# Kernel tuning notes

Hardware: AMD Instinct MI355X
Metric: run time of the kernel (lower is better)

Reference implementation:

```python
import jax, jax.numpy as jnp
import numpy as np

HEADS = 8
DH = 160
LN_EPS = 1e-5


def _ln(x):
    m = jnp.mean(x, axis=-1, keepdims=True)
    v = jnp.var(x, axis=-1, keepdims=True)
    return (x - m) * jax.lax.rsqrt(v + LN_EPS)


def _adaln(x, table, w, b, t):
    # table[t]: [dim]; emb -> [2*dim]; chunk along dim 0 (scalar timestep)
    emb = jax.nn.silu(table[t]) @ w + b
    scale, shift = jnp.split(emb, 2)
    return _ln(x) * (1.0 + scale) + shift


def _attn(x, ctx, wq, wk, wv, wo, bo):
    B, S, _ = x.shape
    Sk = ctx.shape[1]
    q = (x @ wq).reshape(B, S, HEADS, DH).transpose(0, 2, 1, 3)    # [B,H,S,dh]
    k = (ctx @ wk).reshape(B, Sk, HEADS, DH).transpose(0, 2, 1, 3)
    v = (ctx @ wv).reshape(B, Sk, HEADS, DH).transpose(0, 2, 1, 3)
    scores = jnp.einsum('bhid,bhjd->bhij', q, k) * (DH ** -0.5)
    probs = jax.nn.softmax(scores, axis=-1)
    o = jnp.einsum('bhij,bhjd->bhid', probs, v)
    o = o.transpose(0, 2, 1, 3).reshape(B, S, HEADS * DH)
    return o @ wo + bo


def _ff(x, w1, b1, w2, b2):
    h, gate = jnp.split(x @ w1 + b1, 2, axis=-1)
    return (h * jax.nn.gelu(gate, approximate=False)) @ w2 + b2


def setup_inputs() -> dict:
    key = jax.random.key(0)
    ks = jax.random.split(key, 24)
    B, S, SC, DIM, CROSS, INNER = 2, 2048, 77, 1280, 768, 5120

    def w(k, shape, s=0.02):
        return jax.random.normal(k, shape, jnp.float32) * s

    return {
        'hidden_states': jax.random.normal(ks[0], (B, S, DIM), jnp.float32),
        'context': jax.random.normal(ks[1], (B, SC, CROSS), jnp.float32),
        'ada1_emb': w(ks[2], (1000, DIM)),
        'ada1_w': w(ks[3], (DIM, 2 * DIM)),
        'ada1_b': jnp.zeros((2 * DIM,), jnp.float32),
        'ada2_emb': w(ks[4], (1000, DIM)),
        'ada2_w': w(ks[5], (DIM, 2 * DIM)),
        'ada2_b': jnp.zeros((2 * DIM,), jnp.float32),
        'a1_wq': w(ks[6], (DIM, DIM)), 'a1_wk': w(ks[7], (DIM, DIM)),
        'a1_wv': w(ks[8], (DIM, DIM)), 'a1_wo': w(ks[9], (DIM, DIM)),
        'a1_bo': jnp.zeros((DIM,), jnp.float32),
        'a2_wq': w(ks[10], (DIM, DIM)), 'a2_wk': w(ks[11], (CROSS, DIM)),
        'a2_wv': w(ks[12], (CROSS, DIM)), 'a2_wo': w(ks[13], (DIM, DIM)),
        'a2_bo': jnp.zeros((DIM,), jnp.float32),
        'norm3_g': jnp.ones((DIM,), jnp.float32),
        'norm3_b': jnp.zeros((DIM,), jnp.float32),
        'ff_w1': w(ks[14], (DIM, 2 * INNER)),
        'ff_b1': jnp.zeros((2 * INNER,), jnp.float32),
        'ff_w2': w(ks[15], (INNER, DIM)),
        'ff_b2': jnp.zeros((DIM,), jnp.float32),
        'timestep': 500,
    }


def reference(hidden_states, context, ada1_emb, ada1_w, ada1_b, ada2_emb, ada2_w, ada2_b,
              a1_wq, a1_wk, a1_wv, a1_wo, a1_bo, a2_wq, a2_wk, a2_wv, a2_wo, a2_bo,
              norm3_g, norm3_b, ff_w1, ff_b1, ff_w2, ff_b2, timestep):
    x = hidden_states
    # self-attention with AdaLayerNorm
    h = _adaln(x, ada1_emb, ada1_w, ada1_b, timestep)
    x = x + _attn(h, h, a1_wq, a1_wk, a1_wv, a1_wo, a1_bo)
    # cross-attention with AdaLayerNorm
    h = _adaln(x, ada2_emb, ada2_w, ada2_b, timestep)
    x = x + _attn(h, context, a2_wq, a2_wk, a2_wv, a2_wo, a2_bo)
    # feed-forward with affine LayerNorm
    h = _ln(x) * norm3_g + norm3_b
    x = x + _ff(h, ff_w1, ff_b1, ff_w2, ff_b2)
    return x
```

## Files before the change

kernel.cpp:

```cpp
#include <hip/hip_runtime.h>

typedef __attribute__((ext_vector_type(8))) unsigned short ushort8;
typedef __attribute__((ext_vector_type(4))) float f32x4;
typedef __attribute__((ext_vector_type(8))) __bf16 bf16x8;
typedef unsigned short u16;

__device__ inline unsigned short f2bf(float f) {
  unsigned u = __float_as_uint(f);
  unsigned r = (u + 0x7fffu + ((u >> 16) & 1u)) >> 16;
  return (unsigned short)r;
}
__device__ inline float bf2f(unsigned short h) {
  return __uint_as_float(((unsigned)h) << 16);
}

__device__ __forceinline__ void gload_lds16(const void* g, void* l) {
  __builtin_amdgcn_global_load_lds(
      (const __attribute__((address_space(1))) void*)g,
      (__attribute__((address_space(3))) void*)l, 16, 0, 0);
}

__device__ __forceinline__ void decomp_bid(int nbx, int nby, int& z, int& bx, int& by) {
  int bid = blockIdx.x;
  const int nwg = gridDim.x;
  const int q8 = nwg >> 3, r8 = nwg & 7;
  const int xcd = bid & 7, i = bid >> 3;
  bid = (xcd < r8 ? xcd * (q8 + 1) : r8 * (q8 + 1) + (xcd - r8) * q8) + i;
  const int nbb = nbx * nby;
  z = bid / nbb;
  int rem = bid - z * nbb;
  if ((nby & 7) == 0) {
    const int chunk = nbx << 3;
    const int c = rem / chunk, w = rem - c * chunk;
    bx = w >> 3;
    by = (c << 3) + (w & 7);
  } else {
    by = rem / nbx;
    bx = rem - by * nbx;
  }
}

__global__ __launch_bounds__(512, 2) void flash_self(
    const u16* __restrict__ qkv, const u16* __restrict__ vtg, u16* __restrict__ o)
{
  __shared__ __align__(128) u16 Qs[128 * 168];
  __shared__ __align__(128) u16 Ks[2][64 * 168];
  __shared__ __align__(128) u16 Vs[2][160 * 64];
  __shared__ __align__(128) u16 Ps[128 * 64];

  const int tid = threadIdx.x;
  const int lane = tid & 63, wave = tid >> 6;
  const int r15 = lane & 15, kq = lane >> 4;
  const int z = blockIdx.x >> 4, qt = blockIdx.x & 15;
  const int b = z >> 3, hh = z & 7;
  const u16* Qg = qkv + ((long)(b * 2048 + qt * 128)) * 3840 + hh * 160;
  const u16* Kg = qkv + ((long)(b * 2048)) * 3840 + 1280 + hh * 160;
  const u16* Vg = vtg + (long)z * 160 * 2048;

  for (int c = tid; c < 2560; c += 512) {
    const int r = c / 20, e = (c % 20) * 8;
    *(ushort8*)&Qs[r * 168 + e] = *(const ushort8*)(Qg + (long)r * 3840 + e);
  }
  const int c0 = tid, c1 = tid + 512, c2 = tid + 1024;
  const bool has2 = (c2 < 1280);
  const int kR0 = c0 / 20, kE0 = (c0 % 20) * 8;
  const int kR1 = c1 / 20, kE1 = (c1 % 20) * 8;
  const int kR2 = has2 ? c2 / 20 : 0, kE2 = has2 ? (c2 % 20) * 8 : 0;
  const int vR0 = c0 >> 3, vG0 = c0 & 7;
  const int vR1 = c1 >> 3, vG1 = c1 & 7;
  const int vR2 = has2 ? (c2 >> 3) : 0, vG2 = has2 ? (c2 & 7) : 0;

  {
    ushort8 k0 = *(const ushort8*)(Kg + (long)kR0 * 3840 + kE0);
    ushort8 k1 = *(const ushort8*)(Kg + (long)kR1 * 3840 + kE1);
    ushort8 v0 = *(const ushort8*)(Vg + (long)vR0 * 2048 + vG0 * 8);
    ushort8 v1 = *(const ushort8*)(Vg + (long)vR1 * 2048 + vG1 * 8);
    *(ushort8*)&Ks[0][kR0 * 168 + kE0] = k0;
    *(ushort8*)&Ks[0][kR1 * 168 + kE1] = k1;
    *(ushort8*)&Vs[0][vR0 * 64 + ((vG0 ^ (vR0 & 7)) * 8)] = v0;
    *(ushort8*)&Vs[0][vR1 * 64 + ((vG1 ^ (vR1 & 7)) * 8)] = v1;
    if (has2) {
      ushort8 k2 = *(const ushort8*)(Kg + (long)kR2 * 3840 + kE2);
      ushort8 v2 = *(const ushort8*)(Vg + (long)vR2 * 2048 + vG2 * 8);
      *(ushort8*)&Ks[0][kR2 * 168 + kE2] = k2;
      *(ushort8*)&Vs[0][vR2 * 64 + ((vG2 ^ (vR2 & 7)) * 8)] = v2;
    }
  }
  __syncthreads();

  bf16x8 qf[5];
#pragma unroll
  for (int kf = 0; kf < 5; ++kf)
    qf[kf] = *(const bf16x8*)&Qs[(wave * 16 + r15) * 168 + kf * 32 + kq * 8];

  float m[4], l[4] = {0.f, 0.f, 0.f, 0.f};
#pragma unroll
  for (int t = 0; t < 4; ++t) m[t] = -1e30f;
  f32x4 accO[10] = {};
  const float SC = 0.07905694150420949f;

  ushort8 kr0, kr1, kr2, vr0, vr1, vr2;

  for (int step = 0; step < 32; ++step) {
    const int cur = step & 1;
    const bool nl = step < 31;
    if (nl) {
      const long kv1 = (long)(step + 1) * 64;
      kr0 = *(const ushort8*)(Kg + (kv1 + kR0) * 3840 + kE0);
      kr1 = *(const ushort8*)(Kg + (kv1 + kR1) * 3840 + kE1);
      vr0 = *(const ushort8*)(Vg + (long)vR0 * 2048 + kv1 + vG0 * 8);
      vr1 = *(const ushort8*)(Vg + (long)vR1 * 2048 + kv1 + vG1 * 8);
      if (has2) {
        kr2 = *(const ushort8*)(Kg + (kv1 + kR2) * 3840 + kE2);
        vr2 = *(const ushort8*)(Vg + (long)vR2 * 2048 + kv1 + vG2 * 8);
      }
    }
    f32x4 sa[4] = {};
#pragma unroll
    for (int nf = 0; nf < 4; ++nf)
#pragma unroll
      for (int kf = 0; kf < 5; ++kf) {
        const bf16x8 kfrag =
            *(const bf16x8*)&Ks[cur][(nf * 16 + r15) * 168 + kf * 32 + kq * 8];
        sa[nf] = __builtin_amdgcn_mfma_f32_16x16x32_bf16(qf[kf], kfrag, sa[nf], 0, 0, 0);
      }
    float corr[4];
#pragma unroll
    for (int t = 0; t < 4; ++t) {
      float tm = fmaxf(fmaxf(sa[0][t], sa[1][t]), fmaxf(sa[2][t], sa[3][t])) * SC;
      tm = fmaxf(tm, __shfl_xor(tm, 1, 64));
      tm = fmaxf(tm, __shfl_xor(tm, 2, 64));
      tm = fmaxf(tm, __shfl_xor(tm, 4, 64));
      tm = fmaxf(tm, __shfl_xor(tm, 8, 64));
      const float mn = fmaxf(m[t], tm);
      corr[t] = __expf(m[t] - mn);
      m[t] = mn;
    }
    const int qr0 = wave * 16 + kq * 4;
#pragma unroll
    for (int t = 0; t < 4; ++t) {
      float rs = 0.f;
      const int qr = qr0 + t;
#pragma unroll
      for (int nf = 0; nf < 4; ++nf) {
        const float p = __expf(sa[nf][t] * SC - m[t]);
        rs += p;
        const int col = r15 + nf * 16;
        Ps[qr * 64 + (((col >> 3) ^ (qr & 7)) * 8) + (col & 7)] = f2bf(p);
      }
      rs += __shfl_xor(rs, 1, 64);
      rs += __shfl_xor(rs, 2, 64);
      rs += __shfl_xor(rs, 4, 64);
      rs += __shfl_xor(rs, 8, 64);
      l[t] = l[t] * corr[t] + rs;
    }
#pragma unroll
    for (int j = 0; j < 10; ++j)
#pragma unroll
      for (int t = 0; t < 4; ++t) accO[j][t] *= corr[t];
    if (nl) {
      const int nxt = cur ^ 1;
      *(ushort8*)&Ks[nxt][kR0 * 168 + kE0] = kr0;
      *(ushort8*)&Ks[nxt][kR1 * 168 + kE1] = kr1;
      *(ushort8*)&Vs[nxt][vR0 * 64 + ((vG0 ^ (vR0 & 7)) * 8)] = vr0;
      *(ushort8*)&Vs[nxt][vR1 * 64 + ((vG1 ^ (vR1 & 7)) * 8)] = vr1;
      if (has2) {
        *(ushort8*)&Ks[nxt][kR2 * 168 + kE2] = kr2;
        *(ushort8*)&Vs[nxt][vR2 * 64 + ((vG2 ^ (vR2 & 7)) * 8)] = vr2;
      }
    }
    __syncthreads();
    const int arow = wave * 16 + r15;
    bf16x8 pf[2];
#pragma unroll
    for (int k2 = 0; k2 < 2; ++k2)
      pf[k2] = *(const bf16x8*)&Ps[arow * 64 + (((k2 * 4 + kq) ^ (arow & 7)) * 8)];
#pragma unroll
    for (int j = 0; j < 10; ++j)
#pragma unroll
      for (int k2 = 0; k2 < 2; ++k2) {
        const int vrow = j * 16 + r15;
        const bf16x8 vf =
            *(const bf16x8*)&Vs[cur][vrow * 64 + (((k2 * 4 + kq) ^ (vrow & 7)) * 8)];
        accO[j] = __builtin_amdgcn_mfma_f32_16x16x32_bf16(pf[k2], vf, accO[j], 0, 0, 0);
      }
    __syncthreads();
  }
  float inv[4];
#pragma unroll
  for (int t = 0; t < 4; ++t) inv[t] = 1.f / l[t];
  u16* orow = o + ((long)(b * 2048 + qt * 128)) * 1280 + hh * 160;
#pragma unroll
  for (int j = 0; j < 10; ++j)
#pragma unroll
    for (int t = 0; t < 4; ++t) {
      const int qr = wave * 16 + kq * 4 + t;
      orow[(long)qr * 1280 + j * 16 + r15] = f2bf(accO[j][t] * inv[t]);
    }
}

__global__ __launch_bounds__(512, 4) void gemm64(
    const u16* __restrict__ A, long lda, long sAo, long sAi,
    const u16* __restrict__ B, long ldb, long sBo, long sBi,
    void* __restrict__ C, long ldc, long sCo, long sCi,
    const float* __restrict__ bias, const float* __restrict__ resid, long ldr,
    int M, int N, int K, int nbx, int Hdiv, float alpha, int outF32)
{
  __shared__ __align__(128) char smem[65536];
  const int tid = threadIdx.x;
  const int lane = tid & 63, wave = tid >> 6;

  int z, bx, by;
  decomp_bid(nbx, M >> 7, z, bx, by);
  const int m0 = by << 7, n0 = bx << 7;
  const int zb = z / Hdiv, zh = z - zb * Hdiv;
  const u16* Ab = A + (long)zb * sAo + (long)zh * sAi;
  const u16* Bb = B + (long)zb * sBo + (long)zh * sBi;

  const int srow = tid >> 3;
  const int g8 = ((tid & 7) ^ (srow & 7)) * 8;
  long aoff[2], boff[2];
#pragma unroll
  for (int i = 0; i < 2; ++i) {
    aoff[i] = (long)(m0 + i * 64 + srow) * lda + g8;
    boff[i] = (long)(n0 + i * 64 + srow) * ldb + g8;
  }
  const int ldst = tid * 16;

  const int wm = (wave >> 2) * 64, wn = (wave & 3) * 32;
  const int r15 = lane & 15, kq = lane >> 4;
  const int offK0 = (kq ^ (lane & 7)) * 16;
  const int offK1 = ((4 + kq) ^ (lane & 7)) * 16;

  const int nt = K >> 6;

#define STAGE64(bufofs, k0)                                                       \
  do {                                                                            \
    _Pragma("unroll") for (int i = 0; i < 2; ++i)                                 \
        gload_lds16(Ab + aoff[i] + (k0), smem + (bufofs) + i * 8192 + ldst);      \
    _Pragma("unroll") for (int i = 0; i < 2; ++i)                                 \
        gload_lds16(Bb + boff[i] + (k0), smem + (bufofs) + 16384 + i * 8192 + ldst); \
  } while (0)

  STAGE64(0, 0);
  STAGE64(32768, 64);

  f32x4 acc[4][2] = {};

  for (int t = 0; t < nt; ++t) {
    const int cbuf = (t & 1) << 15;
    if (t < nt - 1) asm volatile("s_waitcnt vmcnt(4)" ::: "memory");
    else            asm volatile("s_waitcnt vmcnt(0)" ::: "memory");
    __builtin_amdgcn_s_barrier();

    bf16x8 bfr[2][2];
#pragma unroll
    for (int q = 0; q < 2; ++q) {
      if (q == 0) {
#pragma unroll
        for (int j = 0; j < 2; ++j) {
          const int bb = cbuf + 16384 + (wn + j * 16 + r15) * 128;
          bfr[j][0] = *(const bf16x8*)(smem + bb + offK0);
          bfr[j][1] = *(const bf16x8*)(smem + bb + offK1);
        }
      }
      bf16x8 af[2][2];
#pragma unroll
      for (int i2 = 0; i2 < 2; ++i2) {
        const int ab = cbuf + (wm + (q * 2 + i2) * 16 + r15) * 128;
        af[i2][0] = *(const bf16x8*)(smem + ab + offK0);
        af[i2][1] = *(const bf16x8*)(smem + ab + offK1);
      }
      __builtin_amdgcn_s_setprio(1);
#pragma unroll
      for (int kk = 0; kk < 2; ++kk)
#pragma unroll
        for (int i2 = 0; i2 < 2; ++i2)
#pragma unroll
          for (int j = 0; j < 2; ++j)
            acc[q * 2 + i2][j] = __builtin_amdgcn_mfma_f32_16x16x32_bf16(
                af[i2][kk], bfr[j][kk], acc[q * 2 + i2][j], 0, 0, 0);
      __builtin_amdgcn_s_setprio(0);
      __builtin_amdgcn_s_barrier();
    }
    if (t + 2 < nt) STAGE64(cbuf, (long)(t + 2) * 64);
  }
#undef STAGE64

  const long cbase = (long)zb * sCo + (long)zh * sCi;
  const int rb = (lane >> 4) * 4;
#pragma unroll
  for (int i = 0; i < 4; ++i) {
#pragma unroll
    for (int j = 0; j < 2; ++j) {
      const int gcol = n0 + wn + j * 16 + r15;
      if (gcol >= N) continue;
      const float bv = bias ? bias[gcol] : 0.f;
#pragma unroll
      for (int tt = 0; tt < 4; ++tt) {
        const int grow = m0 + wm + i * 16 + rb + tt;
        float val = acc[i][j][tt] * alpha + bv;
        if (resid) val += resid[(long)grow * ldr + gcol];
        const long cidx = cbase + (long)grow * ldc + gcol;
        if (outF32) ((float*)C)[cidx] = val;
        else ((u16*)C)[cidx] = f2bf(val);
      }
    }
  }
}

__global__ __launch_bounds__(512, 4) void gemm32(
    const u16* __restrict__ A, long lda, long sAo, long sAi,
    const u16* __restrict__ B, long ldb, long sBo, long sBi,
    void* __restrict__ C, long ldc, long sCo, long sCi,
    const float* __restrict__ bias, const float* __restrict__ resid, long ldr,
    int M, int N, int K, int nbx, int Hdiv, float alpha, int outF32)
{
  __shared__ __align__(128) char smem[32768];
  const int tid = threadIdx.x;
  const int lane = tid & 63, wave = tid >> 6;

  int z, bx, by;
  decomp_bid(nbx, M >> 7, z, bx, by);
  const int m0 = by << 7, n0 = bx << 7;
  const int zb = z / Hdiv, zh = z - zb * Hdiv;
  const u16* Ab = A + (long)zb * sAo + (long)zh * sAi;
  const u16* Bb = B + (long)zb * sBo + (long)zh * sBi;

  const int srow = tid >> 2;
  const int g8 = ((tid & 3) ^ ((tid >> 3) & 3)) * 8;
  const long aoff = (long)(m0 + srow) * lda + g8;
  const long boff = (long)(n0 + srow) * ldb + g8;
  const int ldst = tid * 16;

  const int wm = (wave >> 2) * 64, wn = (wave & 3) * 32;
  const int r15 = lane & 15, kq = lane >> 4;
  const int goff = (kq ^ ((r15 >> 1) & 3)) * 16;

  const int nt = K >> 5;

#define STAGE32(bufofs, k0)                                                \
  do {                                                                     \
    gload_lds16(Ab + aoff + (k0), smem + (bufofs) + ldst);                 \
    gload_lds16(Bb + boff + (k0), smem + (bufofs) + 8192 + ldst);          \
  } while (0)

  STAGE32(0, 0);
  STAGE32(16384, 32);

  f32x4 acc[4][2] = {};

  for (int t = 0; t < nt; ++t) {
    const int cbuf = (t & 1) << 14;
    if (t < nt - 1) asm volatile("s_waitcnt vmcnt(2)" ::: "memory");
    else            asm volatile("s_waitcnt vmcnt(0)" ::: "memory");
    __builtin_amdgcn_s_barrier();

    bf16x8 af[4], bfr[2];
#pragma unroll
    for (int i = 0; i < 4; ++i)
      af[i] = *(const bf16x8*)(smem + cbuf + (wm + i * 16 + r15) * 64 + goff);
#pragma unroll
    for (int j = 0; j < 2; ++j)
      bfr[j] = *(const bf16x8*)(smem + cbuf + 8192 + (wn + j * 16 + r15) * 64 + goff);

    __builtin_amdgcn_s_setprio(1);
#pragma unroll
    for (int i = 0; i < 4; ++i)
#pragma unroll
      for (int j = 0; j < 2; ++j)
        acc[i][j] = __builtin_amdgcn_mfma_f32_16x16x32_bf16(af[i], bfr[j], acc[i][j], 0, 0, 0);
    __builtin_amdgcn_s_setprio(0);
    __builtin_amdgcn_s_barrier();

    if (t + 2 < nt) STAGE32(cbuf, (long)(t + 2) * 32);
  }
#undef STAGE32

  const long cbase = (long)zb * sCo + (long)zh * sCi;
  const int rb = (lane >> 4) * 4;
#pragma unroll
  for (int i = 0; i < 4; ++i) {
#pragma unroll
    for (int j = 0; j < 2; ++j) {
      const int gcol = n0 + wn + j * 16 + r15;
      if (gcol >= N) continue;
      const float bv = bias ? bias[gcol] : 0.f;
#pragma unroll
      for (int tt = 0; tt < 4; ++tt) {
        const int grow = m0 + wm + i * 16 + rb + tt;
        float val = acc[i][j][tt] * alpha + bv;
        if (resid) val += resid[(long)grow * ldr + gcol];
        const long cidx = cbase + (long)grow * ldc + gcol;
        if (outF32) ((float*)C)[cidx] = val;
        else ((u16*)C)[cidx] = f2bf(val);
      }
    }
  }
}

__global__ __launch_bounds__(256) void gemm_nt(
    const u16* __restrict__ A, long lda, long sAo, long sAi,
    const u16* __restrict__ B, long ldb, long sBo, long sBi,
    void* __restrict__ C, long ldc, long sCo, long sCi,
    const float* __restrict__ bias,
    const float* __restrict__ resid, long ldr,
    int M, int N, int K, int Hdiv, float alpha, int outF32)
{
  __shared__ u16 As[128 * 32];
  __shared__ u16 Bs[128 * 32];
  const int tid = threadIdx.x;
  const int z = blockIdx.z;
  const int zb = z / Hdiv, zh = z % Hdiv;
  const u16* Ab = A + (long)zb * sAo + (long)zh * sAi;
  const u16* Bb = B + (long)zb * sBo + (long)zh * sBi;
  const long cbase = (long)zb * sCo + (long)zh * sCi;
  const int m0 = blockIdx.y * 128, n0 = blockIdx.x * 128;
  const int lane = tid & 63, wave = tid >> 6;
  const int wm = (wave >> 1) * 64, wn = (wave & 1) * 64;
  const int r15 = lane & 15, kb = (lane >> 4) * 8;

  f32x4 acc[4][4] = {};

  for (int k0 = 0; k0 < K; k0 += 32) {
#pragma unroll
    for (int it = 0; it < 2; ++it) {
      const int c = tid + it * 256;
      const int row = c >> 2, ko = (c & 3) * 8;
      ushort8 va = {0, 0, 0, 0, 0, 0, 0, 0};
      const int gm = m0 + row;
      if (gm < M) va = *reinterpret_cast<const ushort8*>(Ab + (long)gm * lda + k0 + ko);
      *reinterpret_cast<ushort8*>(&As[row * 32 + ko]) = va;
      ushort8 vb = {0, 0, 0, 0, 0, 0, 0, 0};
      const int gn = n0 + row;
      if (gn < N) vb = *reinterpret_cast<const ushort8*>(Bb + (long)gn * ldb + k0 + ko);
      *reinterpret_cast<ushort8*>(&Bs[row * 32 + ko]) = vb;
    }
    __syncthreads();
    bf16x8 af[4], bfr[4];
#pragma unroll
    for (int i = 0; i < 4; ++i)
      af[i] = *reinterpret_cast<const bf16x8*>(&As[(wm + i * 16 + r15) * 32 + kb]);
#pragma unroll
    for (int j = 0; j < 4; ++j)
      bfr[j] = *reinterpret_cast<const bf16x8*>(&Bs[(wn + j * 16 + r15) * 32 + kb]);
#pragma unroll
    for (int i = 0; i < 4; ++i)
#pragma unroll
      for (int j = 0; j < 4; ++j)
        acc[i][j] = __builtin_amdgcn_mfma_f32_16x16x32_bf16(af[i], bfr[j], acc[i][j], 0, 0, 0);
    __syncthreads();
  }

  const int rb = (lane >> 4) * 4;
#pragma unroll
  for (int i = 0; i < 4; ++i) {
#pragma unroll
    for (int j = 0; j < 4; ++j) {
      const int gcol = n0 + wn + j * 16 + r15;
      if (gcol >= N) continue;
#pragma unroll
      for (int t = 0; t < 4; ++t) {
        const int grow = m0 + wm + i * 16 + rb + t;
        if (grow >= M) continue;
        float val = acc[i][j][t] * alpha;
        if (bias) val += bias[gcol];
        if (resid) val += resid[(long)grow * ldr + gcol];
        const long cidx = cbase + (long)grow * ldc + gcol;
        if (outF32) ((float*)C)[cidx] = val;
        else ((u16*)C)[cidx] = f2bf(val);
      }
    }
  }
}

__global__ void transpose_convert(const float* __restrict__ in,
                                  u16* __restrict__ out, int R, int C) {
  __shared__ float tile[32][33];
  const int c0 = blockIdx.x * 32, r0 = blockIdx.y * 32;
  const int tx = threadIdx.x, ty = threadIdx.y;
  for (int i = ty; i < 32; i += 8) {
    const int r = r0 + i, c = c0 + tx;
    tile[i][tx] = (r < R && c < C) ? in[(long)r * C + c] : 0.f;
  }
  __syncthreads();
  for (int i = ty; i < 32; i += 8) {
    const int c = c0 + i, r = r0 + tx;
    if (c < C && r < R) out[(long)c * R + r] = f2bf(tile[tx][i]);
  }
}

__global__ void convert_bf16(const float* __restrict__ in,
                             u16* __restrict__ out, long n) {
  const long i = (long)blockIdx.x * 256 + threadIdx.x;
  if (i < n) out[i] = f2bf(in[i]);
}

__global__ __launch_bounds__(256) void adaln_emb(
    const float* __restrict__ t1, const float* __restrict__ w1, const float* __restrict__ b1,
    const float* __restrict__ t2, const float* __restrict__ w2, const float* __restrict__ b2,
    const int* __restrict__ tstep, float* __restrict__ e1, float* __restrict__ e2)
{
  const int which = blockIdx.y;
  const float* tb = which ? t2 : t1;
  const float* w = which ? w2 : w1;
  const float* bb = which ? b2 : b1;
  float* out = which ? e2 : e1;
  const int t = tstep[0];
  __shared__ float sil[1280];
  const int tid = threadIdx.x;
  for (int i = tid; i < 1280; i += 256) {
    const float xv = tb[(long)t * 1280 + i];
    sil[i] = xv / (1.f + expf(-xv));
  }
  __syncthreads();
  const int j = blockIdx.x * 256 + tid;
  float acc = bb[j];
  for (int k = 0; k < 1280; ++k) acc += sil[k] * w[(long)k * 2560 + j];
  out[j] = acc;
}

__global__ __launch_bounds__(256) void ln_mod(
    const float* __restrict__ x, u16* __restrict__ out,
    const float* __restrict__ emb, const float* __restrict__ g,
    const float* __restrict__ bv, int affine)
{
  const long row = blockIdx.x;
  const float* xr = x + row * 1280;
  const int tid = threadIdx.x;
  float v[5], s = 0.f, s2 = 0.f;
#pragma unroll
  for (int i = 0; i < 5; ++i) {
    const float t = xr[tid + i * 256];
    v[i] = t; s += t; s2 += t * t;
  }
  __shared__ float rs_[4], rs2_[4], bc[2];
  for (int off = 32; off; off >>= 1) {
    s += __shfl_down(s, off, 64);
    s2 += __shfl_down(s2, off, 64);
  }
  if ((tid & 63) == 0) { rs_[tid >> 6] = s; rs2_[tid >> 6] = s2; }
  __syncthreads();
  if (tid == 0) {
    const float S = rs_[0] + rs_[1] + rs_[2] + rs_[3];
    const float S2 = rs2_[0] + rs2_[1] + rs2_[2] + rs2_[3];
    const float mean = S * (1.f / 1280.f);
    const float var = S2 * (1.f / 1280.f) - mean * mean;
    bc[0] = mean; bc[1] = rsqrtf(var + 1e-5f);
  }
  __syncthreads();
  const float mean = bc[0], rstd = bc[1];
#pragma unroll
  for (int i = 0; i < 5; ++i) {
    const int c = tid + i * 256;
    const float ln = (v[i] - mean) * rstd;
    const float y = affine ? (ln * g[c] + bv[c]) : (ln * (1.f + emb[c]) + emb[1280 + c]);
    out[row * 1280 + c] = f2bf(y);
  }
}

__global__ void transpose_v_self(const u16* __restrict__ v, int ldv,
                                 u16* __restrict__ vt) {
  __shared__ u16 t[32][33];
  const int z = blockIdx.z, b = z >> 3, hh = z & 7;
  const int s0 = blockIdx.x * 32, d0 = blockIdx.y * 32;
  const int tx = threadIdx.x, ty = threadIdx.y;
  for (int i = ty; i < 32; i += 8) {
    const int d = d0 + tx;
    t[i][tx] = (d < 160) ? v[((long)(b * 2048 + s0 + i)) * ldv + hh * 160 + d]
                         : (u16)0;
  }
  __syncthreads();
  for (int i = ty; i < 32; i += 8) {
    const int d = d0 + i;
    if (d < 160) vt[((long)z * 160 + d) * 2048 + s0 + tx] = t[tx][i];
  }
}

__global__ void make_vct(const u16* __restrict__ vc,
                         u16* __restrict__ vct) {
  const int idx = blockIdx.x * 256 + threadIdx.x;
  if (idx >= 16 * 160 * 96) return;
  const int s = idx % 96;
  const int d = (idx / 96) % 160;
  const int z = idx / (96 * 160);
  const int b = z >> 3, hh = z & 7;
  u16 val = 0;
  if (s < 77) val = vc[((long)(b * 77 + s)) * 2560 + hh * 160 + d];
  vct[idx] = val;
}

__global__ __launch_bounds__(64) void softmax_cross(u16* __restrict__ S) {
  const long row = blockIdx.x;
  u16* p = S + row * 96;
  const int tid = threadIdx.x;
  const float v0 = (tid < 77) ? bf2f(p[tid]) : -1e30f;
  const float v1 = (tid + 64 < 77) ? bf2f(p[tid + 64]) : -1e30f;
  float mx = fmaxf(v0, v1);
  for (int off = 32; off; off >>= 1) mx = fmaxf(mx, __shfl_down(mx, off, 64));
  mx = __shfl(mx, 0, 64);
  const float e0 = (tid < 77) ? expf(v0 - mx) : 0.f;
  const float e1 = (tid + 64 < 77) ? expf(v1 - mx) : 0.f;
  float s = e0 + e1;
  for (int off = 32; off; off >>= 1) s += __shfl_down(s, off, 64);
  s = __shfl(s, 0, 64);
  const float inv = 1.f / s;
  p[tid] = (tid < 77) ? f2bf(e0 * inv) : (u16)0;
  if (tid + 64 < 96) p[tid + 64] = (tid + 64 < 77) ? f2bf(e1 * inv) : (u16)0;
}

__global__ __launch_bounds__(256) void geglu(const u16* __restrict__ ff1,
                                             u16* __restrict__ out) {
  const long gid = (long)blockIdx.x * 256 + threadIdx.x;
  if (gid >= (long)4096 * 640) return;
  const long i = gid / 640;
  const int jb = (int)(gid % 640) * 8;
  const ushort8 a = *reinterpret_cast<const ushort8*>(ff1 + i * 10240 + jb);
  const ushort8 gt = *reinterpret_cast<const ushort8*>(ff1 + i * 10240 + 5120 + jb);
  ushort8 o;
#pragma unroll
  for (int e = 0; e < 8; ++e) {
    const float av = bf2f(a[e]);
    const float gv = bf2f(gt[e]);
    const float gel = 0.5f * gv * (1.f + erff(gv * 0.7071067811865475f));
    o[e] = f2bf(av * gel);
  }
  *reinterpret_cast<ushort8*>(out + i * 5120 + jb) = o;
}

extern "C" void kernel_launch(void* const* d_in, const int* in_sizes, int n_in,
                              void* d_out, int out_size, void* d_ws, size_t ws_size,
                              hipStream_t stream) {
  (void)in_sizes; (void)n_in; (void)out_size; (void)ws_size;

  const float* hidden   = (const float*)d_in[0];
  const float* context  = (const float*)d_in[1];
  const float* ada1_tab = (const float*)d_in[2];
  const float* ada1_w   = (const float*)d_in[3];
  const float* ada1_b   = (const float*)d_in[4];
  const float* ada2_tab = (const float*)d_in[5];
  const float* ada2_w   = (const float*)d_in[6];
  const float* ada2_b   = (const float*)d_in[7];
  const float* a1_wq = (const float*)d_in[8];
  const float* a1_wk = (const float*)d_in[9];
  const float* a1_wv = (const float*)d_in[10];
  const float* a1_wo = (const float*)d_in[11];
  const float* a1_bo = (const float*)d_in[12];
  const float* a2_wq = (const float*)d_in[13];
  const float* a2_wk = (const float*)d_in[14];
  const float* a2_wv = (const float*)d_in[15];
  const float* a2_wo = (const float*)d_in[16];
  const float* a2_bo = (const float*)d_in[17];
  const float* n3_g  = (const float*)d_in[18];
  const float* n3_b  = (const float*)d_in[19];
  const float* ff_w1 = (const float*)d_in[20];
  const float* ff_b1 = (const float*)d_in[21];
  const float* ff_w2 = (const float*)d_in[22];
  const float* ff_b2 = (const float*)d_in[23];
  const int*   tstep = (const int*)d_in[24];
  float* xout = (float*)d_out;

  char* base = (char*)d_ws;
  size_t off = 0;
  auto alloc = [&](size_t bytes) -> void* {
    void* p = base + off;
    off = (off + bytes + 255) & ~(size_t)255;
    return p;
  };
  u16* wqkvT = (u16*)alloc((size_t)3 * 1280 * 1280 * 2);
  u16* wo1T = (u16*)alloc((size_t)1280 * 1280 * 2);
  u16* wq2T = (u16*)alloc((size_t)1280 * 1280 * 2);
  u16* wkv2T = (u16*)alloc((size_t)2 * 1280 * 768 * 2);
  u16* wo2T = (u16*)alloc((size_t)1280 * 1280 * 2);
  u16* w1T  = (u16*)alloc((size_t)10240 * 1280 * 2);
  u16* w2T  = (u16*)alloc((size_t)1280 * 5120 * 2);
  u16* ctxb = (u16*)alloc((size_t)154 * 768 * 2);
  float* emb1 = (float*)alloc(2560 * 4);
  float* emb2 = (float*)alloc(2560 * 4);
  u16* h   = (u16*)alloc((size_t)4096 * 1280 * 2);
  u16* qkv = (u16*)alloc((size_t)4096 * 3840 * 2);
  u16* vt  = (u16*)alloc((size_t)16 * 160 * 2048 * 2);
  u16* vct = (u16*)alloc((size_t)16 * 160 * 96 * 2);
  u16* o   = (u16*)alloc((size_t)4096 * 1280 * 2);
  u16* scores = (u16*)alloc((size_t)16 * 2048 * 96 * 2);
  u16* qc = qkv;
  u16* kvc = o;
  u16* ffh = qkv;
  u16* ff1out = (u16*)alloc((size_t)4096 * 10240 * 2);

  auto g64 = [&](const u16* A, long lda, long sAo, long sAi,
                 const u16* B, long ldb, long sBo, long sBi,
                 void* C, long ldc, long sCo, long sCi,
                 const float* bias, const float* resid, long ldr,
                 int M, int N, int K, int batch, int Hdiv, float alpha, int outF32) {
    const int nbx = (N + 127) >> 7;
    const int nwg = nbx * (M >> 7) * batch;
    gemm64<<<nwg, 512, 0, stream>>>(A, lda, sAo, sAi, B, ldb, sBo, sBi,
                                    C, ldc, sCo, sCi, bias, resid, ldr,
                                    M, N, K, nbx, Hdiv, alpha, outF32);
  };
  auto g32 = [&](const u16* A, long lda, long sAo, long sAi,
                 const u16* B, long ldb, long sBo, long sBi,
                 void* C, long ldc, long sCo, long sCi,
                 const float* bias, const float* resid, long ldr,
                 int M, int N, int K, int batch, int Hdiv, float alpha, int outF32) {
    const int nbx = (N + 127) >> 7;
    const int nwg = nbx * (M >> 7) * batch;
    gemm32<<<nwg, 512, 0, stream>>>(A, lda, sAo, sAi, B, ldb, sBo, sBi,
                                    C, ldc, sCo, sCi, bias, resid, ldr,
                                    M, N, K, nbx, Hdiv, alpha, outF32);
  };
  auto gemm = [&](const u16* A, long lda, long sAo, long sAi,
                  const u16* B, long ldb, long sBo, long sBi,
                  void* C, long ldc, long sCo, long sCi,
                  const float* bias, const float* resid, long ldr,
                  int M, int N, int K, int batch, int Hdiv, float alpha, int outF32) {
    dim3 g((N + 127) / 128, (M + 127) / 128, batch);
    gemm_nt<<<g, 256, 0, stream>>>(A, lda, sAo, sAi, B, ldb, sBo, sBi, C, ldc, sCo, sCi,
                                   bias, resid, ldr, M, N, K, Hdiv, alpha, outF32);
  };
  auto tconv = [&](const float* in, u16* out, int R, int C) {
    transpose_convert<<<dim3((C + 31) / 32, (R + 31) / 32), dim3(32, 8), 0, stream>>>(in, out, R, C);
  };

  tconv(a1_wq, wqkvT, 1280, 1280);
  tconv(a1_wk, wqkvT + (size_t)1280 * 1280, 1280, 1280);
  tconv(a1_wv, wqkvT + (size_t)2 * 1280 * 1280, 1280, 1280);
  tconv(a1_wo, wo1T, 1280, 1280);
  tconv(a2_wq, wq2T, 1280, 1280);
  tconv(a2_wk, wkv2T, 768, 1280);
  tconv(a2_wv, wkv2T + (size_t)1280 * 768, 768, 1280);
  tconv(a2_wo, wo2T, 1280, 1280);
  tconv(ff_w1, w1T, 1280, 10240);
  tconv(ff_w2, w2T, 5120, 1280);
  {
    const long n = (long)154 * 768;
    convert_bf16<<<(int)((n + 255) / 256), 256, 0, stream>>>(context, ctxb, n);
  }
  adaln_emb<<<dim3(10, 2), 256, 0, stream>>>(ada1_tab, ada1_w, ada1_b,
                                             ada2_tab, ada2_w, ada2_b, tstep, emb1, emb2);

  const float ascale = 0.07905694150420949f;
  u16* qc_ = qc;
  u16* vs = qkv + 2560;

  ln_mod<<<4096, 256, 0, stream>>>(hidden, h, emb1, nullptr, nullptr, 0);
  g64(h, 1280, 0, 0, wqkvT, 1280, 0, 0, qkv, 3840, 0, 0,
      nullptr, nullptr, 0, 4096, 3840, 1280, 1, 1, 1.f, 0);
  transpose_v_self<<<dim3(64, 5, 16), dim3(32, 8), 0, stream>>>(vs, 3840, vt);
  flash_self<<<256, 512, 0, stream>>>(qkv, vt, o);
  g64(o, 1280, 0, 0, wo1T, 1280, 0, 0, xout, 1280, 0, 0,
      a1_bo, hidden, 1280, 4096, 1280, 1280, 1, 1, 1.f, 1);

  ln_mod<<<4096, 256, 0, stream>>>(xout, h, emb2, nullptr, nullptr, 0);
  g64(h, 1280, 0, 0, wq2T, 1280, 0, 0, qc_, 1280, 0, 0,
      nullptr, nullptr, 0, 4096, 1280, 1280, 1, 1, 1.f, 0);
  gemm(ctxb, 768, 0, 0, wkv2T, 768, 0, 0, kvc, 2560, 0, 0, nullptr, nullptr, 0,
       154, 2560, 768, 1, 1, 1.f, 0);
  make_vct<<<(16 * 160 * 96 + 255) / 256, 256, 0, stream>>>(kvc + 1280, vct);
  g32(qc_, 1280, (long)2048 * 1280, 160, kvc, 2560, (long)77 * 2560, 160,
      scores, 96, (long)8 * 2048 * 96, (long)2048 * 96, nullptr, nullptr, 0,
      2048, 77, 160, 16, 8, ascale, 0);
  softmax_cross<<<16 * 2048, 64, 0, stream>>>(scores);
  g32(scores, 96, (long)8 * 2048 * 96, (long)2048 * 96,
      vct, 96, (long)8 * 160 * 96, (long)160 * 96,
      o, 1280, (long)2048 * 1280, 160, nullptr, nullptr, 0,
      2048, 160, 96, 16, 8, 1.f, 0);
  g64(o, 1280, 0, 0, wo2T, 1280, 0, 0, xout, 1280, 0, 0,
      a2_bo, xout, 1280, 4096, 1280, 1280, 1, 1, 1.f, 1);

  ln_mod<<<4096, 256, 0, stream>>>(xout, h, nullptr, n3_g, n3_b, 1);
  g64(h, 1280, 0, 0, w1T, 1280, 0, 0, ff1out, 10240, 0, 0,
      ff_b1, nullptr, 0, 4096, 10240, 1280, 1, 1, 1.f, 0);
  geglu<<<(int)(((long)4096 * 640 + 255) / 256), 256, 0, stream>>>(ff1out, ffh);
  g64(ffh, 5120, 0, 0, w2T, 5120, 0, 0, xout, 1280, 0, 0,
      ff_b2, xout, 1280, 4096, 1280, 5120, 1, 1, 1.f, 1);
}
```

Baseline: 718.8 us.

## Fuse cross-attention into one kernel and GEGLU into FF1 GEMM epilogue

```diff
diff --git a/kernel.cpp b/kernel.cpp
--- a/kernel.cpp
+++ b/kernel.cpp
@@ -199,12 +199,118 @@
     }
 }
 
+__global__ __launch_bounds__(512, 1) void flash_cross(
+    const u16* __restrict__ q, const u16* __restrict__ kv, u16* __restrict__ o)
+{
+  __shared__ __align__(128) u16 Qs[128 * 168];
+  __shared__ __align__(128) u16 Ks[80 * 168];
+  __shared__ __align__(128) u16 Vts[160 * 104];
+  __shared__ __align__(128) u16 Ps[128 * 104];
+
+  const int tid = threadIdx.x;
+  const int lane = tid & 63, wave = tid >> 6;
+  const int r15 = lane & 15, kq = lane >> 4;
+  const int z = blockIdx.x >> 4, qt = blockIdx.x & 15;
+  const int b = z >> 3, hh = z & 7;
+  const u16* Qg = q + ((long)(b * 2048 + qt * 128)) * 1280 + hh * 160;
+  const u16* Kg = kv + (long)b * 77 * 2560 + hh * 160;
+  const u16* Vg = Kg + 1280;
+
+  for (int c = tid; c < 2560; c += 512) {
+    const int r = c / 20, e = (c % 20) * 8;
+    *(ushort8*)&Qs[r * 168 + e] = *(const ushort8*)(Qg + (long)r * 1280 + e);
+  }
+  for (int c = tid; c < 1540; c += 512) {
+    const int r = c / 20, e = (c % 20) * 8;
+    *(ushort8*)&Ks[r * 168 + e] = *(const ushort8*)(Kg + (long)r * 2560 + e);
+  }
+  for (int c = tid; c < 3 * 168; c += 512) Ks[77 * 168 + c] = 0;
+  for (int c = tid; c < 77 * 160; c += 512) {
+    const int s = c / 160, d = c - s * 160;
+    Vts[d * 104 + s] = Vg[(long)s * 2560 + d];
+  }
+  for (int c = tid; c < 160 * 27; c += 512) {
+    const int d = c / 27, cc = 77 + (c - d * 27);
+    Vts[d * 104 + cc] = 0;
+  }
+  for (int c = tid; c < 128 * 16; c += 512) {
+    const int r = c >> 4, cc = 80 + (c & 15);
+    Ps[r * 104 + cc] = 0;
+  }
+  __syncthreads();
+
+  const float SC = 0.07905694150420949f;
+  bf16x8 qf[5];
+#pragma unroll
+  for (int kf = 0; kf < 5; ++kf)
+    qf[kf] = *(const bf16x8*)&Qs[(wave * 16 + r15) * 168 + kf * 32 + kq * 8];
+  f32x4 sa[5] = {};
+#pragma unroll
+  for (int nf = 0; nf < 5; ++nf)
+#pragma unroll
+    for (int kf = 0; kf < 5; ++kf) {
+      const bf16x8 kfrag = *(const bf16x8*)&Ks[(nf * 16 + r15) * 168 + kf * 32 + kq * 8];
+      sa[nf] = __builtin_amdgcn_mfma_f32_16x16x32_bf16(qf[kf], kfrag, sa[nf], 0, 0, 0);
+    }
+  float inv[4];
+#pragma unroll
+  for (int t = 0; t < 4; ++t) {
+    float sv[5];
+    float m = -1e30f;
+#pragma unroll
+    for (int nf = 0; nf < 5; ++nf) {
+      const int col = nf * 16 + r15;
+      sv[nf] = (col < 77) ? sa[nf][t] * SC : -1e30f;
+      m = fmaxf(m, sv[nf]);
+    }
+    m = fmaxf(m, __shfl_xor(m, 1, 64));
+    m = fmaxf(m, __shfl_xor(m, 2, 64));
+    m = fmaxf(m, __shfl_xor(m, 4, 64));
+    m = fmaxf(m, __shfl_xor(m, 8, 64));
+    const int qr = wave * 16 + kq * 4 + t;
+    float rs = 0.f;
+#pragma unroll
+    for (int nf = 0; nf < 5; ++nf) {
+      const float p = __expf(sv[nf] - m);
+      rs += p;
+      Ps[qr * 104 + nf * 16 + r15] = f2bf(p);
+    }
+    rs += __shfl_xor(rs, 1, 64);
+    rs += __shfl_xor(rs, 2, 64);
+    rs += __shfl_xor(rs, 4, 64);
+    rs += __shfl_xor(rs, 8, 64);
+    inv[t] = 1.f / rs;
+  }
+  __syncthreads();
+  const int arow = wave * 16 + r15;
+  bf16x8 pf[3];
+#pragma unroll
+  for (int k2 = 0; k2 < 3; ++k2)
+    pf[k2] = *(const bf16x8*)&Ps[arow * 104 + k2 * 32 + kq * 8];
+  f32x4 accO[10] = {};
+#pragma unroll
+  for (int j = 0; j < 10; ++j)
+#pragma unroll
+    for (int k2 = 0; k2 < 3; ++k2) {
+      const bf16x8 vf = *(const bf16x8*)&Vts[(j * 16 + r15) * 104 + k2 * 32 + kq * 8];
+      accO[j] = __builtin_amdgcn_mfma_f32_16x16x32_bf16(pf[k2], vf, accO[j], 0, 0, 0);
+    }
+  u16* orow = o + ((long)(b * 2048 + qt * 128)) * 1280 + hh * 160;
+#pragma unroll
+  for (int j = 0; j < 10; ++j)
+#pragma unroll
+    for (int t = 0; t < 4; ++t) {
+      const int qr = wave * 16 + kq * 4 + t;
+      orow[(long)qr * 1280 + j * 16 + r15] = f2bf(accO[j][t] * inv[t]);
+    }
+}
+
 __global__ __launch_bounds__(512, 4) void gemm64(
     const u16* __restrict__ A, long lda, long sAo, long sAi,
     const u16* __restrict__ B, long ldb, long sBo, long sBi,
     void* __restrict__ C, long ldc, long sCo, long sCi,
     const float* __restrict__ bias, const float* __restrict__ resid, long ldr,
-    int M, int N, int K, int nbx, int Hdiv, float alpha, int outF32)
+    int M, int N, int K, int nbx, int Hdiv, float alpha, int outF32, int geglu)
 {
   __shared__ __align__(128) char smem[65536];
   const int tid = threadIdx.x;
@@ -289,96 +395,23 @@
 
   const long cbase = (long)zb * sCo + (long)zh * sCi;
   const int rb = (lane >> 4) * 4;
-#pragma unroll
-  for (int i = 0; i < 4; ++i) {
-#pragma unroll
-    for (int j = 0; j < 2; ++j) {
-      const int gcol = n0 + wn + j * 16 + r15;
-      if (gcol >= N) continue;
-      const float bv = bias ? bias[gcol] : 0.f;
+  if (geglu) {
+    const int cH = n0 + wn + r15;
+    const float bh = bias[cH], bg = bias[cH + 16];
+    const int ocol = ((n0 + wn) >> 1) + r15;
+#pragma unroll
+    for (int i = 0; i < 4; ++i) {
 #pragma unroll
       for (int tt = 0; tt < 4; ++tt) {
         const int grow = m0 + wm + i * 16 + rb + tt;
-        float val = acc[i][j][tt] * alpha + bv;
-        if (resid) val += resid[(long)grow * ldr + gcol];
-        const long cidx = cbase + (long)grow * ldc + gcol;
-        if (outF32) ((float*)C)[cidx] = val;
-        else ((u16*)C)[cidx] = f2bf(val);
-      }
-    }
-  }
-}
-
-__global__ __launch_bounds__(512, 4) void gemm32(
-    const u16* __restrict__ A, long lda, long sAo, long sAi,
-    const u16* __restrict__ B, long ldb, long sBo, long sBi,
-    void* __restrict__ C, long ldc, long sCo, long sCi,
-    const float* __restrict__ bias, const float* __restrict__ resid, long ldr,
-    int M, int N, int K, int nbx, int Hdiv, float alpha, int outF32)
-{
-  __shared__ __align__(128) char smem[32768];
-  const int tid = threadIdx.x;
-  const int lane = tid & 63, wave = tid >> 6;
-
-  int z, bx, by;
-  decomp_bid(nbx, M >> 7, z, bx, by);
-  const int m0 = by << 7, n0 = bx << 7;
-  const int zb = z / Hdiv, zh = z - zb * Hdiv;
-  const u16* Ab = A + (long)zb * sAo + (long)zh * sAi;
-  const u16* Bb = B + (long)zb * sBo + (long)zh * sBi;
-
-  const int srow = tid >> 2;
-  const int g8 = ((tid & 3) ^ ((tid >> 3) & 3)) * 8;
-  const long aoff = (long)(m0 + srow) * lda + g8;
-  const long boff = (long)(n0 + srow) * ldb + g8;
-  const int ldst = tid * 16;
-
-  const int wm = (wave >> 2) * 64, wn = (wave & 3) * 32;
-  const int r15 = lane & 15, kq = lane >> 4;
-  const int goff = (kq ^ ((r15 >> 1) & 3)) * 16;
-
-  const int nt = K >> 5;
-
-#define STAGE32(bufofs, k0)                                                \
-  do {                                                                     \
-    gload_lds16(Ab + aoff + (k0), smem + (bufofs) + ldst);                 \
-    gload_lds16(Bb + boff + (k0), smem + (bufofs) + 8192 + ldst);          \
-  } while (0)
-
-  STAGE32(0, 0);
-  STAGE32(16384, 32);
-
-  f32x4 acc[4][2] = {};
-
-  for (int t = 0; t < nt; ++t) {
-    const int cbuf = (t & 1) << 14;
-    if (t < nt - 1) asm volatile("s_waitcnt vmcnt(2)" ::: "memory");
-    else            asm volatile("s_waitcnt vmcnt(0)" ::: "memory");
-    __builtin_amdgcn_s_barrier();
-
-    bf16x8 af[4], bfr[2];
-#pragma unroll
-    for (int i = 0; i < 4; ++i)
-      af[i] = *(const bf16x8*)(smem + cbuf + (wm + i * 16 + r15) * 64 + goff);
-#pragma unroll
-    for (int j = 0; j < 2; ++j)
-      bfr[j] = *(const bf16x8*)(smem + cbuf + 8192 + (wn + j * 16 + r15) * 64 + goff);
-
-    __builtin_amdgcn_s_setprio(1);
-#pragma unroll
-    for (int i = 0; i < 4; ++i)
-#pragma unroll
-      for (int j = 0; j < 2; ++j)
-        acc[i][j] = __builtin_amdgcn_mfma_f32_16x16x32_bf16(af[i], bfr[j], acc[i][j], 0, 0, 0);
-    __builtin_amdgcn_s_setprio(0);
-    __builtin_amdgcn_s_barrier();
-
-    if (t + 2 < nt) STAGE32(cbuf, (long)(t + 2) * 32);
-  }
-#undef STAGE32
-
-  const long cbase = (long)zb * sCo + (long)zh * sCi;
-  const int rb = (lane >> 4) * 4;
+        const float hv = acc[i][0][tt] + bh;
+        const float gv = acc[i][1][tt] + bg;
+        const float gel = 0.5f * gv * (1.f + erff(gv * 0.7071067811865475f));
+        ((u16*)C)[(long)grow * ldc + ocol] = f2bf(hv * gel);
+      }
+    }
+    return;
+  }
 #pragma unroll
   for (int i = 0; i < 4; ++i) {
 #pragma unroll
@@ -490,6 +523,27 @@
   }
 }
 
+__global__ void tconv_ff1(const float* __restrict__ in, u16* __restrict__ out) {
+  __shared__ float tile[32][33];
+  const int r0 = blockIdx.y * 32;
+  const int k0 = blockIdx.x * 32;
+  const int w = r0 >> 5;
+  const int tx = threadIdx.x, ty = threadIdx.y;
+  const int src = (tx < 16) ? (w * 16 + tx) : (5120 + w * 16 + tx - 16);
+  for (int i = ty; i < 32; i += 8)
+    tile[i][tx] = in[(long)(k0 + i) * 10240 + src];
+  __syncthreads();
+  for (int i = ty; i < 32; i += 8)
+    out[(long)(r0 + i) * 1280 + k0 + tx] = f2bf(tile[tx][i]);
+}
+
+__global__ void perm_b1(const float* __restrict__ b, float* __restrict__ bp) {
+  const int r = blockIdx.x * 256 + threadIdx.x;
+  if (r >= 10240) return;
+  const int w = r >> 5, s = r & 31;
+  bp[r] = b[(s < 16) ? (w * 16 + s) : (5120 + w * 16 + s - 16)];
+}
+
 __global__ void convert_bf16(const float* __restrict__ in,
                              u16* __restrict__ out, long n) {
   const long i = (long)blockIdx.x * 256 + threadIdx.x;
@@ -575,57 +629,6 @@
     const int d = d0 + i;
     if (d < 160) vt[((long)z * 160 + d) * 2048 + s0 + tx] = t[tx][i];
   }
-}
-
-__global__ void make_vct(const u16* __restrict__ vc,
-                         u16* __restrict__ vct) {
-  const int idx = blockIdx.x * 256 + threadIdx.x;
-  if (idx >= 16 * 160 * 96) return;
-  const int s = idx % 96;
-  const int d = (idx / 96) % 160;
-  const int z = idx / (96 * 160);
-  const int b = z >> 3, hh = z & 7;
-  u16 val = 0;
-  if (s < 77) val = vc[((long)(b * 77 + s)) * 2560 + hh * 160 + d];
-  vct[idx] = val;
-}
-
-__global__ __launch_bounds__(64) void softmax_cross(u16* __restrict__ S) {
-  const long row = blockIdx.x;
-  u16* p = S + row * 96;
-  const int tid = threadIdx.x;
-  const float v0 = (tid < 77) ? bf2f(p[tid]) : -1e30f;
-  const float v1 = (tid + 64 < 77) ? bf2f(p[tid + 64]) : -1e30f;
-  float mx = fmaxf(v0, v1);
-  for (int off = 32; off; off >>= 1) mx = fmaxf(mx, __shfl_down(mx, off, 64));
-  mx = __shfl(mx, 0, 64);
-  const float e0 = (tid < 77) ? expf(v0 - mx) : 0.f;
-  const float e1 = (tid + 64 < 77) ? expf(v1 - mx) : 0.f;
-  float s = e0 + e1;
-  for (int off = 32; off; off >>= 1) s += __shfl_down(s, off, 64);
-  s = __shfl(s, 0, 64);
-  const float inv = 1.f / s;
-  p[tid] = (tid < 77) ? f2bf(e0 * inv) : (u16)0;
-  if (tid + 64 < 96) p[tid + 64] = (tid + 64 < 77) ? f2bf(e1 * inv) : (u16)0;
-}
-
-__global__ __launch_bounds__(256) void geglu(const u16* __restrict__ ff1,
-                                             u16* __restrict__ out) {
-  const long gid = (long)blockIdx.x * 256 + threadIdx.x;
-  if (gid >= (long)4096 * 640) return;
-  const long i = gid / 640;
-  const int jb = (int)(gid % 640) * 8;
-  const ushort8 a = *reinterpret_cast<const ushort8*>(ff1 + i * 10240 + jb);
-  const ushort8 gt = *reinterpret_cast<const ushort8*>(ff1 + i * 10240 + 5120 + jb);
-  ushort8 o;
-#pragma unroll
-  for (int e = 0; e < 8; ++e) {
-    const float av = bf2f(a[e]);
-    const float gv = bf2f(gt[e]);
-    const float gel = 0.5f * gv * (1.f + erff(gv * 0.7071067811865475f));
-    o[e] = f2bf(av * gel);
-  }
-  *reinterpret_cast<ushort8*>(out + i * 5120 + jb) = o;
 }
 
 extern "C" void kernel_launch(void* const* d_in, const int* in_sizes, int n_in,
@@ -672,43 +675,31 @@
   u16* wq2T = (u16*)alloc((size_t)1280 * 1280 * 2);
   u16* wkv2T = (u16*)alloc((size_t)2 * 1280 * 768 * 2);
   u16* wo2T = (u16*)alloc((size_t)1280 * 1280 * 2);
-  u16* w1T  = (u16*)alloc((size_t)10240 * 1280 * 2);
+  u16* w1Tp = (u16*)alloc((size_t)10240 * 1280 * 2);
   u16* w2T  = (u16*)alloc((size_t)1280 * 5120 * 2);
   u16* ctxb = (u16*)alloc((size_t)154 * 768 * 2);
   float* emb1 = (float*)alloc(2560 * 4);
   float* emb2 = (float*)alloc(2560 * 4);
+  float* b1p  = (float*)alloc(10240 * 4);
   u16* h   = (u16*)alloc((size_t)4096 * 1280 * 2);
   u16* qkv = (u16*)alloc((size_t)4096 * 3840 * 2);
   u16* vt  = (u16*)alloc((size_t)16 * 160 * 2048 * 2);
-  u16* vct = (u16*)alloc((size_t)16 * 160 * 96 * 2);
   u16* o   = (u16*)alloc((size_t)4096 * 1280 * 2);
-  u16* scores = (u16*)alloc((size_t)16 * 2048 * 96 * 2);
+  u16* kvx = (u16*)alloc((size_t)154 * 2560 * 2);
   u16* qc = qkv;
-  u16* kvc = o;
   u16* ffh = qkv;
-  u16* ff1out = (u16*)alloc((size_t)4096 * 10240 * 2);
 
   auto g64 = [&](const u16* A, long lda, long sAo, long sAi,
                  const u16* B, long ldb, long sBo, long sBi,
                  void* C, long ldc, long sCo, long sCi,
                  const float* bias, const float* resid, long ldr,
-                 int M, int N, int K, int batch, int Hdiv, float alpha, int outF32) {
+                 int M, int N, int K, int batch, int Hdiv, float alpha,
+                 int outF32, int geglu) {
     const int nbx = (N + 127) >> 7;
     const int nwg = nbx * (M >> 7) * batch;
     gemm64<<<nwg, 512, 0, stream>>>(A, lda, sAo, sAi, B, ldb, sBo, sBi,
                                     C, ldc, sCo, sCi, bias, resid, ldr,
-                                    M, N, K, nbx, Hdiv, alpha, outF32);
-  };
-  auto g32 = [&](const u16* A, long lda, long sAo, long sAi,
-                 const u16* B, long ldb, long sBo, long sBi,
-                 void* C, long ldc, long sCo, long sCi,
-                 const float* bias, const float* resid, long ldr,
-                 int M, int N, int K, int batch, int Hdiv, float alpha, int outF32) {
-    const int nbx = (N + 127) >> 7;
-    const int nwg = nbx * (M >> 7) * batch;
-    gemm32<<<nwg, 512, 0, stream>>>(A, lda, sAo, sAi, B, ldb, sBo, sBi,
-                                    C, ldc, sCo, sCi, bias, resid, ldr,
-                                    M, N, K, nbx, Hdiv, alpha, outF32);
+                                    M, N, K, nbx, Hdiv, alpha, outF32, geglu);
   };
   auto gemm = [&](const u16* A, long lda, long sAo, long sAi,
                   const u16* B, long ldb, long sBo, long sBi,
@@ -731,7 +722,8 @@
   tconv(a2_wk, wkv2T, 768, 1280);
   tconv(a2_wv, wkv2T + (size_t)1280 * 768, 768, 1280);
   tconv(a2_wo, wo2T, 1280, 1280);
-  tconv(ff_w1, w1T, 1280, 10240);
+  tconv_ff1<<<dim3(40, 320), dim3(32, 8), 0, stream>>>(ff_w1, w1Tp);
+  perm_b1<<<40, 256, 0, stream>>>(ff_b1, b1p);
   tconv(ff_w2, w2T, 5120, 1280);
   {
     const long n = (long)154 * 768;
@@ -740,39 +732,28 @@
   adaln_emb<<<dim3(10, 2), 256, 0, stream>>>(ada1_tab, ada1_w, ada1_b,
                                              ada2_tab, ada2_w, ada2_b, tstep, emb1, emb2);
 
-  const float ascale = 0.07905694150420949f;
-  u16* qc_ = qc;
   u16* vs = qkv + 2560;
 
   ln_mod<<<4096, 256, 0, stream>>>(hidden, h, emb1, nullptr, nullptr, 0);
   g64(h, 1280, 0, 0, wqkvT, 1280, 0, 0, qkv, 3840, 0, 0,
-      nullptr, nullptr, 0, 4096, 3840, 1280, 1, 1, 1.f, 0);
+      nullptr, nullptr, 0, 4096, 3840, 1280, 1, 1, 1.f, 0, 0);
   transpose_v_self<<<dim3(64, 5, 16), dim3(32, 8), 0, stream>>>(vs, 3840, vt);
   flash_self<<<256, 512, 0, stream>>>(qkv, vt, o);
   g64(o, 1280, 0, 0, wo1T, 1280, 0, 0, xout, 1280, 0, 0,
-      a1_bo, hidden, 1280, 4096, 1280, 1280, 1, 1, 1.f, 1);
+      a1_bo, hidden, 1280, 4096, 1280, 1280, 1, 1, 1.f, 1, 0);
 
   ln_mod<<<4096, 256, 0, stream>>>(xout, h, emb2, nullptr, nullptr, 0);
-  g64(h, 1280, 0, 0, wq2T, 1280, 0, 0, qc_, 1280, 0, 0,
-      nullptr, nullptr, 0, 4096, 1280, 1280, 1, 1, 1.f, 0);
-  gemm(ctxb, 768, 0, 0, wkv2T, 768, 0, 0, kvc, 2560, 0, 0, nullptr, nullptr, 0,
+  g64(h, 1280, 0, 0, wq2T, 1280, 0, 0, qc, 1280, 0, 0,
+      nullptr, nullptr, 0, 4096, 1280, 1280, 1, 1, 1.f, 0, 0);
+  gemm(ctxb, 768, 0, 0, wkv2T, 768, 0, 0, kvx, 2560, 0, 0, nullptr, nullptr, 0,
        154, 2560, 768, 1, 1, 1.f, 0);
-  make_vct<<<(16 * 160 * 96 + 255) / 256, 256, 0, stream>>>(kvc + 1280, vct);
-  g32(qc_, 1280, (long)2048 * 1280, 160, kvc, 2560, (long)77 * 2560, 160,
-      scores, 96, (long)8 * 2048 * 96, (long)2048 * 96, nullptr, nullptr, 0,
-      2048, 77, 160, 16, 8, ascale, 0);
-  softmax_cross<<<16 * 2048, 64, 0, stream>>>(scores);
-  g32(scores, 96, (long)8 * 2048 * 96, (long)2048 * 96,
-      vct, 96, (long)8 * 160 * 96, (long)160 * 96,
-      o, 1280, (long)2048 * 1280, 160, nullptr, nullptr, 0,
-      2048, 160, 96, 16, 8, 1.f, 0);
+  flash_cross<<<256, 512, 0, stream>>>(qc, kvx, o);
   g64(o, 1280, 0, 0, wo2T, 1280, 0, 0, xout, 1280, 0, 0,
-      a2_bo, xout, 1280, 4096, 1280, 1280, 1, 1, 1.f, 1);
+      a2_bo, xout, 1280, 4096, 1280, 1280, 1, 1, 1.f, 1, 0);
 
   ln_mod<<<4096, 256, 0, stream>>>(xout, h, nullptr, n3_g, n3_b, 1);
-  g64(h, 1280, 0, 0, w1T, 1280, 0, 0, ff1out, 10240, 0, 0,
-      ff_b1, nullptr, 0, 4096, 10240, 1280, 1, 1, 1.f, 0);
-  geglu<<<(int)(((long)4096 * 640 + 255) / 256), 256, 0, stream>>>(ff1out, ffh);
+  g64(h, 1280, 0, 0, w1Tp, 1280, 0, 0, ffh, 5120, 0, 0,
+      b1p, nullptr, 0, 4096, 10240, 1280, 1, 1, 1.f, 0, 1);
   g64(ffh, 5120, 0, 0, w2T, 5120, 0, 0, xout, 1280, 0, 0,
-      ff_b2, xout, 1280, 4096, 1280, 5120, 1, 1, 1.f, 1);
-}
+      ff_b2, xout, 1280, 4096, 1280, 5120, 1, 1, 1.f, 1, 0);
+}
```

After: 673.6 us, median of 2. 1.07x faster.
